# Optimization experiments

Hardware: AMD Instinct MI355X
Metric: run time of the kernel (lower is better)

## Reference

```python
import jax, jax.numpy as jnp
import numpy as np

N, E = 50000, 800000
IN_DIM, HID, HEADS, OUT = 128, 16, 8, 64
SLOPE = 0.2  # DGL GATConv default negative_slope


def setup_inputs() -> dict:
    key = jax.random.key(0)
    ks = jax.random.split(key, 12)
    return {
        "features": jax.random.normal(ks[0], (N, IN_DIM), jnp.float32),
        "src": jax.random.randint(ks[1], (E,), 0, N, jnp.int32),
        "dst": jax.random.randint(ks[2], (E,), 0, N, jnp.int32),
        "w": jax.random.uniform(ks[3], (E,), jnp.float32),
        "W1": jax.random.normal(ks[4], (IN_DIM, HEADS * HID), jnp.float32) / np.sqrt(IN_DIM),
        "al1": jax.random.normal(ks[5], (HEADS, HID), jnp.float32) * 0.1,
        "ar1": jax.random.normal(ks[6], (HEADS, HID), jnp.float32) * 0.1,
        "b1": jnp.zeros((HEADS * HID,), jnp.float32),
        "W2": jax.random.normal(ks[7], (HEADS * HID, OUT), jnp.float32) / np.sqrt(HEADS * HID),
        "al2": jax.random.normal(ks[8], (1, OUT), jnp.float32) * 0.1,
        "ar2": jax.random.normal(ks[9], (1, OUT), jnp.float32) * 0.1,
        "b2": jnp.zeros((OUT,), jnp.float32),
    }


def _gat_layer(x, src, dst, w, W, al, ar, b, heads, dout, act):
    """DGL GATConv with edge_weight: proj -> edge attn -> edge softmax(dst) -> * w -> scatter-sum."""
    n = x.shape[0]
    h = (x @ W).reshape(n, heads, dout)                 # [N,H,D]
    el = (h * al[None]).sum(-1)                         # [N,H] left attn logits
    er = (h * ar[None]).sum(-1)                         # [N,H] right attn logits
    e = el[src] + er[dst]                               # [E,H]
    e = jnp.where(e > 0, e, SLOPE * e)                  # leaky_relu
    m = jax.ops.segment_max(e, dst, num_segments=n)     # per-dst max for stable softmax
    a = jnp.exp(e - m[dst])
    z = jax.ops.segment_sum(a, dst, num_segments=n)
    a = (a / z[dst]) * w[:, None]                       # edge softmax scaled by edge weight
    msg = a[:, :, None] * h[src]                        # [E,H,D] gathered weighted messages
    rst = jax.ops.segment_sum(msg, dst, num_segments=n) # [N,H,D] scatter aggregation
    rst = rst + b.reshape(1, heads, dout)               # GATConv bias
    return act(rst) if act is not None else rst


def reference(features, src, dst, w, W1, al1, ar1, b1, W2, al2, ar2, b2):
    h = _gat_layer(features, src, dst, w, W1, al1, ar1, b1, HEADS, HID, jax.nn.relu)
    h = jax.nn.relu(h).reshape(N, HEADS * HID)          # outer F.relu + flatten(1)
    out = _gat_layer(h, src, dst, w, W2, al2, ar2, b2, 1, OUT, None)
    return out.squeeze(1)                               # [N,OUT]
```

## Files before the change

kernel.cpp:

```cpp
#include <hip/hip_runtime.h>
#include <hip/hip_fp16.h>

#define NN 50000
#define NE 800000

#define NBK 196
#define BSH 8
#define BMASK 255
#define SCAP 5120
#define CHUNK 2048
#define NBLK_A ((NE + CHUNK - 1) / CHUNK)
#define NBLK_P ((NN + 63) / 64)
#define GPAD 4

typedef _Float16 f16x8 __attribute__((ext_vector_type(8)));
typedef float f32x4 __attribute__((ext_vector_type(4)));

__global__ __launch_bounds__(256) void init_k(const float* __restrict__ W1,
                                              const float* __restrict__ W2,
                                              __half* __restrict__ w1t,
                                              __half* __restrict__ w2t,
                                              int* __restrict__ gcur) {
    const int i = blockIdx.x * 256 + threadIdx.x;
    {
        const int k = i >> 7, n = i & 127;
        w1t[n * 128 + k] = __float2half(W1[i]);
    }
    if (i < 128 * 64) {
        const int k = i >> 6, n = i & 63;
        w2t[n * 128 + k] = __float2half(W2[i]);
    }
    if (i < NBK) gcur[i << GPAD] = 0;
}

__global__ __launch_bounds__(256) void sortA_proj1_k(const int* __restrict__ src,
                                                     const int* __restrict__ dst,
                                                     const float* __restrict__ wE,
                                                     int* __restrict__ gcur,
                                                     int2* __restrict__ stage,
                                                     const float* __restrict__ x,
                                                     const __half* __restrict__ w1t,
                                                     const float* __restrict__ al1,
                                                     const float* __restrict__ ar1,
                                                     __half* __restrict__ h1h,
                                                     float* __restrict__ el1,
                                                     float* __restrict__ er1) {
    const int t = threadIdx.x;
    if (blockIdx.x < NBLK_A) {
        __shared__ int hcnt[NBK], lexcl[NBK], lcur[NBK], gbase[NBK];
        __shared__ int wsum[4];
        __shared__ int2 lbuf[CHUNK];
        const int e0 = blockIdx.x * CHUNK;
        const int ne = min(CHUNK, NE - e0);
        if (t < NBK) { hcnt[t] = 0; lcur[t] = 0; }
        __syncthreads();
        for (int i = t; i < ne; i += 256) atomicAdd(&hcnt[dst[e0 + i] >> BSH], 1);
        __syncthreads();
        {
            const int lane = t & 63, wid = t >> 6;
            const int v = (t < NBK) ? hcnt[t] : 0;
            int s = v;
            #pragma unroll
            for (int off = 1; off < 64; off <<= 1) {
                int u = __shfl_up(s, off, 64);
                if (lane >= off) s += u;
            }
            if (lane == 63) wsum[wid] = s;
            __syncthreads();
            int add = 0;
            for (int w = 0; w < wid; w++) add += wsum[w];
            if (t < NBK) lexcl[t] = s - v + add;
        }
        __syncthreads();
        if (t < NBK && hcnt[t] > 0) gbase[t] = atomicAdd(&gcur[t << GPAD], hcnt[t]);
        __syncthreads();
        for (int i = t; i < ne; i += 256) {
            const int d = dst[e0 + i];
            const int b = d >> BSH;
            const int r = atomicAdd(&lcur[b], 1);
            lbuf[lexcl[b] + r] = make_int2((src[e0 + i] & 0xFFFF) | ((d & BMASK) << 16) | (b << 24),
                                           __float_as_int(wE[e0 + i]));
        }
        __syncthreads();
        for (int i = t; i < ne; i += 256) {
            const int2 v = lbuf[i];
            const int b = (unsigned int)v.x >> 24;
            const int pos = gbase[b] + (i - lexcl[b]);
            stage[(size_t)b * SCAP + pos] = v;
        }
    } else {
        const int bid = blockIdx.x - NBLK_A;
        const int l = t & 63, wv = t >> 6;
        const int rbase = bid * 64 + wv * 16;
        const int cl = l & 15, kg = l >> 4;
        const int arow = rbase + cl;
        const float* xrow = x + (size_t)(arow < NN ? arow : NN - 1) * 128;
        f16x8 afrag[4];
        #pragma unroll
        for (int ks = 0; ks < 4; ks++) {
            const float4 u0 = *(const float4*)(xrow + ks * 32 + kg * 8);
            const float4 u1 = *(const float4*)(xrow + ks * 32 + kg * 8 + 4);
            f16x8 a;
            a[0] = (_Float16)u0.x; a[1] = (_Float16)u0.y; a[2] = (_Float16)u0.z; a[3] = (_Float16)u0.w;
            a[4] = (_Float16)u1.x; a[5] = (_Float16)u1.y; a[6] = (_Float16)u1.z; a[7] = (_Float16)u1.w;
            afrag[ks] = a;
        }
        f32x4 acc[8];
        #pragma unroll
        for (int nt = 0; nt < 8; nt++) { acc[nt][0]=0.f; acc[nt][1]=0.f; acc[nt][2]=0.f; acc[nt][3]=0.f; }
        #pragma unroll
        for (int nt = 0; nt < 8; nt++) {
            const f16x8* bp = (const f16x8*)(w1t + (size_t)(nt * 16 + cl) * 128 + kg * 8);
            #pragma unroll
            for (int ks = 0; ks < 4; ks++)
                acc[nt] = __builtin_amdgcn_mfma_f32_16x16x32_f16(afrag[ks], bp[ks * 4], acc[nt], 0, 0, 0);
        }
        const int orow0 = rbase + kg * 4;
        #pragma unroll
        for (int nt = 0; nt < 8; nt++) {
            const int col = nt * 16 + cl;
            const float alc = al1[col], arc = ar1[col];
            #pragma unroll
            for (int r = 0; r < 4; r++) {
                const float v = acc[nt][r];
                const int orow = orow0 + r;
                const bool ok = (orow < NN);
                if (ok) h1h[(size_t)orow * 128 + col] = __float2half(v);
                float pe = v * alc, pr = v * arc;
                #pragma unroll
                for (int m = 1; m < 16; m <<= 1) {
                    pe += __shfl_xor(pe, m, 64);
                    pr += __shfl_xor(pr, m, 64);
                }
                if (ok && cl == 0) {
                    el1[(size_t)orow * 8 + nt] = pe;
                    er1[(size_t)orow * 8 + nt] = pr;
                }
            }
        }
    }
}

__global__ __launch_bounds__(1024) void sortB_k(const int* __restrict__ gcur,
                                                const int2* __restrict__ stage,
                                                int* __restrict__ offs,
                                                unsigned int* __restrict__ csr) {
    __shared__ int cnt[256], cur[256], gall[NBK];
    __shared__ int wsum[4];
    __shared__ int sbase;
    const int b = blockIdx.x, t = threadIdx.x;
    if (t < NBK) gall[t] = gcur[t << GPAD];
    if (t < 256) cnt[t] = 0;
    __syncthreads();
    const int nb = gall[b];
    if (t < 64) {
        int part = 0;
        for (int i = t; i < b; i += 64) part += gall[i];
        #pragma unroll
        for (int m = 1; m < 64; m <<= 1) part += __shfl_xor(part, m, 64);
        if (t == 0) sbase = part;
    }
    const int2* sp = stage + (size_t)b * SCAP;
    for (int i = t; i < nb; i += 1024) atomicAdd(&cnt[(sp[i].x >> 16) & BMASK], 1);
    __syncthreads();
    const int base = sbase;
    const int dlo = b << BSH;
    {
        const int lane = t & 63, wid = t >> 6;
        const int v = (t < 256) ? cnt[t] : 0;
        int s = v;
        #pragma unroll
        for (int off = 1; off < 64; off <<= 1) {
            int u = __shfl_up(s, off, 64);
            if (lane >= off) s += u;
        }
        if (t < 256 && lane == 63) wsum[wid] = s;
        __syncthreads();
        if (t < 256) {
            int add = 0;
            for (int w = 0; w < wid; w++) add += wsum[w];
            const int excl = s - v + add;
            cur[t] = excl;
            if (dlo + t < NN) offs[dlo + t] = base + excl;
        }
        if (b == NBK - 1 && t == 0) offs[NN] = base + nb;
    }
    __syncthreads();
    for (int i = t; i < nb; i += 1024) {
        const int2 pr = sp[i];
        const int dloc = (pr.x >> 16) & BMASK;
        const int sv = pr.x & 0xFFFF;
        const int r = atomicAdd(&cur[dloc], 1);
        const __half hw = __float2half(__int_as_float(pr.y));
        csr[base + r] = (unsigned int)sv | ((unsigned int)__half_as_ushort(hw) << 16);
    }
}

__global__ __launch_bounds__(128) void agg1_k(const int* __restrict__ offs,
                                              const unsigned int* __restrict__ csr,
                                              const __half* __restrict__ h1h,
                                              const float* __restrict__ el1,
                                              const float* __restrict__ er1,
                                              const float* __restrict__ b1,
                                              __half* __restrict__ h2in_h) {
    const int t = threadIdx.x, w = t >> 6, l = t & 63;
    const int n = blockIdx.x * 2 + w;
    const int beg = offs[n], deg = offs[n + 1] - beg;
    const int h = l & 7, eb = l >> 3;
    const int g = l & 15, es = l >> 4, hg = g >> 1;
    const float er_h = er1[(size_t)n * 8 + h];
    float z_lane = 0.f;
    float acc[8];
    #pragma unroll
    for (int j = 0; j < 8; j++) acc[j] = 0.f;
    const float4* hp4 = (const float4*)h1h;

    int pr = 0;
    if (l < 32 && l < deg) pr = (int)csr[beg + l];
    for (int base = 0; base < deg; base += 32) {
        int prn = 0;
        const int nbase = base + 32;
        if (nbase < deg && l < 32 && nbase + l < deg) prn = (int)csr[beg + nbase + l];
        float pwv[4];
        #pragma unroll
        for (int k = 0; k < 4; k++) {
            const unsigned int pre = (unsigned int)__shfl(pr, eb + 8 * k, 64);
            float lg = -1e30f;
            if (base + eb + 8 * k < deg) {
                const float v = el1[(size_t)(pre & 0xFFFF) * 8 + h] + er_h;
                lg = v > 0.f ? v : 0.2f * v;
            }
            const float p = __expf(lg);
            z_lane += p;
            pwv[k] = p * __half2float(__ushort_as_half((unsigned short)(pre >> 16)));
        }
        int sv[8];
        float pp[8];
        #pragma unroll
        for (int k = 0; k < 8; k++) sv[k] = __shfl(pr, es + 4 * k, 64) & 0xFFFF;
        #pragma unroll
        for (int k = 0; k < 8; k++) {
            const int slane = ((es + 4 * (k & 1)) << 3) | hg;
            pp[k] = __shfl(pwv[k >> 1], slane, 64);
        }
        float4 vv[8];
        #pragma unroll
        for (int k = 0; k < 8; k++) vv[k] = hp4[(size_t)sv[k] * 16 + g];
        #pragma unroll
        for (int k = 0; k < 8; k++) {
            #pragma unroll
            for (int q = 0; q < 4; q++) {
                const float2 f = __half22float2(((const __half2*)&vv[k])[q]);
                acc[2 * q]     = fmaf(pp[k], f.x, acc[2 * q]);
                acc[2 * q + 1] = fmaf(pp[k], f.y, acc[2 * q + 1]);
            }
        }
        pr = prn;
    }
    z_lane += __shfl_xor(z_lane, 8, 64);
    z_lane += __shfl_xor(z_lane, 16, 64);
    z_lane += __shfl_xor(z_lane, 32, 64);
    #pragma unroll
    for (int j = 0; j < 8; j++) {
        acc[j] += __shfl_xor(acc[j], 16, 64);
        acc[j] += __shfl_xor(acc[j], 32, 64);
    }
    const float zg = __shfl(z_lane, hg, 64);
    if (l < 16) {
        const float inv = (deg > 0) ? 1.f / zg : 0.f;
        const float4* b4 = (const float4*)b1;
        const float4 bb0 = b4[g * 2], bb1 = b4[g * 2 + 1];
        __half hv[8];
        hv[0] = __float2half(fmaxf(acc[0] * inv + bb0.x, 0.f));
        hv[1] = __float2half(fmaxf(acc[1] * inv + bb0.y, 0.f));
        hv[2] = __float2half(fmaxf(acc[2] * inv + bb0.z, 0.f));
        hv[3] = __float2half(fmaxf(acc[3] * inv + bb0.w, 0.f));
        hv[4] = __float2half(fmaxf(acc[4] * inv + bb1.x, 0.f));
        hv[5] = __float2half(fmaxf(acc[5] * inv + bb1.y, 0.f));
        hv[6] = __float2half(fmaxf(acc[6] * inv + bb1.z, 0.f));
        hv[7] = __float2half(fmaxf(acc[7] * inv + bb1.w, 0.f));
        *(int4*)(h2in_h + (size_t)n * 128 + g * 8) = *(const int4*)hv;
    }
}

__global__ __launch_bounds__(256) void proj2_k(const __half* __restrict__ xh,
                                               const __half* __restrict__ w2t,
                                               const float* __restrict__ al2,
                                               const float* __restrict__ ar2,
                                               __half* __restrict__ h2h,
                                               float* __restrict__ el2,
                                               float* __restrict__ er2) {
    const int t = threadIdx.x, l = t & 63, wv = t >> 6;
    const int rbase = blockIdx.x * 64 + wv * 16;
    const int cl = l & 15, kg = l >> 4;
    const int arow = rbase + cl;
    const __half* xrow = xh + (size_t)(arow < NN ? arow : NN - 1) * 128;
    f16x8 afrag[4];
    #pragma unroll
    for (int ks = 0; ks < 4; ks++)
        afrag[ks] = *(const f16x8*)(xrow + ks * 32 + kg * 8);
    f32x4 acc[4];
    #pragma unroll
    for (int nt = 0; nt < 4; nt++) { acc[nt][0]=0.f; acc[nt][1]=0.f; acc[nt][2]=0.f; acc[nt][3]=0.f; }
    #pragma unroll
    for (int nt = 0; nt < 4; nt++) {
        const f16x8* bp = (const f16x8*)(w2t + (size_t)(nt * 16 + cl) * 128 + kg * 8);
        #pragma unroll
        for (int ks = 0; ks < 4; ks++)
            acc[nt] = __builtin_amdgcn_mfma_f32_16x16x32_f16(afrag[ks], bp[ks * 4], acc[nt], 0, 0, 0);
    }
    const int orow0 = rbase + kg * 4;
    float pe[4] = {0.f, 0.f, 0.f, 0.f}, pr[4] = {0.f, 0.f, 0.f, 0.f};
    #pragma unroll
    for (int nt = 0; nt < 4; nt++) {
        const int col = nt * 16 + cl;
        const float alc = al2[col], arc = ar2[col];
        #pragma unroll
        for (int r = 0; r < 4; r++) {
            const float v = acc[nt][r];
            const int orow = orow0 + r;
            if (orow < NN) h2h[(size_t)orow * 64 + col] = __float2half(v);
            pe[r] = fmaf(v, alc, pe[r]);
            pr[r] = fmaf(v, arc, pr[r]);
        }
    }
    #pragma unroll
    for (int r = 0; r < 4; r++) {
        #pragma unroll
        for (int m = 1; m < 16; m <<= 1) {
            pe[r] += __shfl_xor(pe[r], m, 64);
            pr[r] += __shfl_xor(pr[r], m, 64);
        }
        const int orow = orow0 + r;
        if (cl == 0 && orow < NN) { el2[orow] = pe[r]; er2[orow] = pr[r]; }
    }
}

__global__ __launch_bounds__(128) void agg2_k(const int* __restrict__ offs,
                                              const unsigned int* __restrict__ csr,
                                              const __half* __restrict__ h2h,
                                              const float* __restrict__ el2,
                                              const float* __restrict__ er2,
                                              const float* __restrict__ b2,
                                              float* __restrict__ out) {
    const int t = threadIdx.x, w = t >> 6, l = t & 63;
    const int n = blockIdx.x * 2 + w;
    const int beg = offs[n], deg = offs[n + 1] - beg;
    const int g = l & 7, es = l >> 3;
    const float erd = er2[n];
    float z_lane = 0.f;
    float acc[8];
    #pragma unroll
    for (int j = 0; j < 8; j++) acc[j] = 0.f;
    const float4* hp4 = (const float4*)h2h;

    int pr = 0;
    if (l < 32 && l < deg) pr = (int)csr[beg + l];
    for (int base = 0; base < deg; base += 32) {
        int prn = 0;
        const int nbase = base + 32;
        if (nbase < deg && l < 32 && nbase + l < deg) prn = (int)csr[beg + nbase + l];
        float pw = 0.f;
        if (l < 32 && base + l < deg) {
            const float v = el2[(unsigned int)pr & 0xFFFF] + erd;
            const float lg = v > 0.f ? v : 0.2f * v;
            const float p = __expf(lg);
            z_lane += p;
            pw = p * __half2float(__ushort_as_half((unsigned short)((unsigned int)pr >> 16)));
        }
        int sv[4];
        float pp[4];
        #pragma unroll
        for (int k = 0; k < 4; k++) {
            sv[k] = __shfl(pr, es + 8 * k, 64) & 0xFFFF;
            pp[k] = __shfl(pw, es + 8 * k, 64);
        }
        float4 vv[4];
        #pragma unroll
        for (int k = 0; k < 4; k++) vv[k] = hp4[(size_t)sv[k] * 8 + g];
        #pragma unroll
        for (int k = 0; k < 4; k++) {
            #pragma unroll
            for (int q = 0; q < 4; q++) {
                const float2 f = __half22float2(((const __half2*)&vv[k])[q]);
                acc[2 * q]     = fmaf(pp[k], f.x, acc[2 * q]);
                acc[2 * q + 1] = fmaf(pp[k], f.y, acc[2 * q + 1]);
            }
        }
        pr = prn;
    }
    z_lane += __shfl_xor(z_lane, 1, 64);
    z_lane += __shfl_xor(z_lane, 2, 64);
    z_lane += __shfl_xor(z_lane, 4, 64);
    z_lane += __shfl_xor(z_lane, 8, 64);
    z_lane += __shfl_xor(z_lane, 16, 64);
    z_lane += __shfl_xor(z_lane, 32, 64);
    #pragma unroll
    for (int j = 0; j < 8; j++) {
        acc[j] += __shfl_xor(acc[j], 8, 64);
        acc[j] += __shfl_xor(acc[j], 16, 64);
        acc[j] += __shfl_xor(acc[j], 32, 64);
    }
    if (l < 8) {
        const float inv = (deg > 0) ? 1.f / z_lane : 0.f;
        const float4* b4 = (const float4*)b2;
        const float4 bb0 = b4[g * 2], bb1 = b4[g * 2 + 1];
        float4 o0, o1;
        o0.x = acc[0] * inv + bb0.x;
        o0.y = acc[1] * inv + bb0.y;
        o0.z = acc[2] * inv + bb0.z;
        o0.w = acc[3] * inv + bb0.w;
        o1.x = acc[4] * inv + bb1.x;
        o1.y = acc[5] * inv + bb1.y;
        o1.z = acc[6] * inv + bb1.z;
        o1.w = acc[7] * inv + bb1.w;
        float4* op = (float4*)(out + (size_t)n * 64 + g * 8);
        op[0] = o0; op[1] = o1;
    }
}


extern "C" void kernel_launch(void* const* d_in, const int* in_sizes, int n_in,
                              void* d_out, int out_size, void* d_ws, size_t ws_size,
                              hipStream_t stream) {
    const float* feat = (const float*)d_in[0];
    const int*   srcv = (const int*)d_in[1];
    const int*   dstv = (const int*)d_in[2];
    const float* wE   = (const float*)d_in[3];
    const float* W1   = (const float*)d_in[4];
    const float* al1  = (const float*)d_in[5];
    const float* ar1  = (const float*)d_in[6];
    const float* b1   = (const float*)d_in[7];
    const float* W2   = (const float*)d_in[8];
    const float* al2  = (const float*)d_in[9];
    const float* ar2  = (const float*)d_in[10];
    const float* b2   = (const float*)d_in[11];
    float* out = (float*)d_out;

    char* ws = (char*)d_ws;
    size_t off = 0;
    auto take = [&](size_t bytes) -> char* {
        char* pp = ws + off;
        off = (off + bytes + 255) & ~(size_t)255;
        return pp;
    };
    __half* h1h   = (__half*)take((size_t)NN * 128 * 2);
    __half* h2h   = (__half*)take((size_t)NN * 64 * 2);
    __half* h2in_h= (__half*)take((size_t)NN * 128 * 2);
    float* el1  = (float*)take((size_t)NN * 8 * 4);
    float* er1  = (float*)take((size_t)NN * 8 * 4);
    float* el2  = (float*)take((size_t)NN * 4);
    float* er2  = (float*)take((size_t)NN * 4);
    int* offs   = (int*)take((size_t)(NN + 1) * 4);
    unsigned int* csr = (unsigned int*)take((size_t)NE * 4);
    int* gcur   = (int*)take((size_t)(NBK << GPAD) * 4);
    __half* w1t = (__half*)take((size_t)128 * 128 * 2);
    __half* w2t = (__half*)take((size_t)64 * 128 * 2);
    int2* stage = (int2*)h2in_h;

    init_k<<<64, 256, 0, stream>>>(W1, W2, w1t, w2t, gcur);
    sortA_proj1_k<<<NBLK_A + NBLK_P, 256, 0, stream>>>(srcv, dstv, wE, gcur, stage,
                                                       feat, w1t, al1, ar1, h1h, el1, er1);
    sortB_k<<<NBK, 1024, 0, stream>>>(gcur, stage, offs, csr);
    agg1_k<<<NN / 2, 128, 0, stream>>>(offs, csr, h1h, el1, er1, b1, h2in_h);
    proj2_k<<<(NN + 63) / 64, 256, 0, stream>>>(h2in_h, w2t, al2, ar2, h2h, el2, er2);
    agg2_k<<<NN / 2, 128, 0, stream>>>(offs, csr, h2h, el2, er2, b2, out);
}
```

Before: 138.0 us.

## Precompute layer-1 edge attention weights and softmax denominators during CSR sort

Moves the layer-1 per-edge exp(leaky_relu(el+er))*w computation into the CSR scatter kernel. It writes per-edge fp16 weights for all 8 heads and per-node denominators, accumulated with shared-memory atomics. The aggregation kernel then just reads the precomputed weights instead of gathering el1 and computing exponentials. This adds an extra per-edge array write and read, and it puts more work into a low-occupancy sort kernel with shared atomic contention.

```diff
diff --git a/kernel.cpp b/kernel.cpp
--- a/kernel.cpp
+++ b/kernel.cpp
@@ -143,14 +143,26 @@
 
 __global__ __launch_bounds__(1024) void sortB_k(const int* __restrict__ gcur,
                                                 const int2* __restrict__ stage,
+                                                const float* __restrict__ el1,
+                                                const float* __restrict__ er1,
                                                 int* __restrict__ offs,
-                                                unsigned int* __restrict__ csr) {
+                                                unsigned int* __restrict__ csr,
+                                                __half* __restrict__ pwh,
+                                                float* __restrict__ zf) {
     __shared__ int cnt[256], cur[256], gall[NBK];
     __shared__ int wsum[4];
     __shared__ int sbase;
+    __shared__ float erl[256][8];
+    __shared__ float zacc[256][8];
     const int b = blockIdx.x, t = threadIdx.x;
+    const int dlo = b << BSH;
     if (t < NBK) gall[t] = gcur[t << GPAD];
     if (t < 256) cnt[t] = 0;
+    for (int i = t; i < 2048; i += 1024) {
+        const int node = dlo + (i >> 3);
+        erl[i >> 3][i & 7] = (node < NN) ? er1[(size_t)node * 8 + (i & 7)] : 0.f;
+        zacc[i >> 3][i & 7] = 0.f;
+    }
     __syncthreads();
     const int nb = gall[b];
     if (t < 64) {
@@ -164,7 +176,6 @@
     for (int i = t; i < nb; i += 1024) atomicAdd(&cnt[(sp[i].x >> 16) & BMASK], 1);
     __syncthreads();
     const int base = sbase;
-    const int dlo = b << BSH;
     {
         const int lane = t & 63, wid = t >> 6;
         const int v = (t < 256) ? cnt[t] : 0;
@@ -190,58 +201,60 @@
         const int2 pr = sp[i];
         const int dloc = (pr.x >> 16) & BMASK;
         const int sv = pr.x & 0xFFFF;
+        const float wf = __int_as_float(pr.y);
         const int r = atomicAdd(&cur[dloc], 1);
-        const __half hw = __float2half(__int_as_float(pr.y));
+        const __half hw = __float2half(wf);
         csr[base + r] = (unsigned int)sv | ((unsigned int)__half_as_ushort(hw) << 16);
+        const float4 e0v = *(const float4*)(el1 + (size_t)sv * 8);
+        const float4 e1v = *(const float4*)(el1 + (size_t)sv * 8 + 4);
+        float elv[8];
+        elv[0]=e0v.x; elv[1]=e0v.y; elv[2]=e0v.z; elv[3]=e0v.w;
+        elv[4]=e1v.x; elv[5]=e1v.y; elv[6]=e1v.z; elv[7]=e1v.w;
+        __half hv[8];
+        #pragma unroll
+        for (int h = 0; h < 8; h++) {
+            float lg = elv[h] + erl[dloc][h];
+            lg = lg > 0.f ? lg : 0.2f * lg;
+            const float p = __expf(lg);
+            atomicAdd(&zacc[dloc][h], p);
+            hv[h] = __float2half(p * wf);
+        }
+        *(int4*)(pwh + (size_t)(base + r) * 8) = *(const int4*)hv;
+    }
+    __syncthreads();
+    for (int i = t; i < 2048; i += 1024) {
+        const int node = dlo + (i >> 3);
+        if (node < NN) zf[(size_t)node * 8 + (i & 7)] = zacc[i >> 3][i & 7];
     }
 }
 
 __global__ __launch_bounds__(128) void agg1_k(const int* __restrict__ offs,
                                               const unsigned int* __restrict__ csr,
+                                              const __half* __restrict__ pwh,
+                                              const float* __restrict__ zf,
                                               const __half* __restrict__ h1h,
-                                              const float* __restrict__ el1,
-                                              const float* __restrict__ er1,
                                               const float* __restrict__ b1,
                                               __half* __restrict__ h2in_h) {
     const int t = threadIdx.x, w = t >> 6, l = t & 63;
     const int n = blockIdx.x * 2 + w;
     const int beg = offs[n], deg = offs[n + 1] - beg;
-    const int h = l & 7, eb = l >> 3;
     const int g = l & 15, es = l >> 4, hg = g >> 1;
-    const float er_h = er1[(size_t)n * 8 + h];
-    float z_lane = 0.f;
     float acc[8];
     #pragma unroll
     for (int j = 0; j < 8; j++) acc[j] = 0.f;
     const float4* hp4 = (const float4*)h1h;
 
-    int pr = 0;
-    if (l < 32 && l < deg) pr = (int)csr[beg + l];
     for (int base = 0; base < deg; base += 32) {
-        int prn = 0;
-        const int nbase = base + 32;
-        if (nbase < deg && l < 32 && nbase + l < deg) prn = (int)csr[beg + nbase + l];
-        float pwv[4];
-        #pragma unroll
-        for (int k = 0; k < 4; k++) {
-            const unsigned int pre = (unsigned int)__shfl(pr, eb + 8 * k, 64);
-            float lg = -1e30f;
-            if (base + eb + 8 * k < deg) {
-                const float v = el1[(size_t)(pre & 0xFFFF) * 8 + h] + er_h;
-                lg = v > 0.f ? v : 0.2f * v;
-            }
-            const float p = __expf(lg);
-            z_lane += p;
-            pwv[k] = p * __half2float(__ushort_as_half((unsigned short)(pre >> 16)));
-        }
         int sv[8];
         float pp[8];
         #pragma unroll
-        for (int k = 0; k < 8; k++) sv[k] = __shfl(pr, es + 4 * k, 64) & 0xFFFF;
-        #pragma unroll
         for (int k = 0; k < 8; k++) {
-            const int slane = ((es + 4 * (k & 1)) << 3) | hg;
-            pp[k] = __shfl(pwv[k >> 1], slane, 64);
+            const int E = es + 4 * k;
+            const bool ok = (base + E < deg);
+            const int idx = beg + base + (ok ? E : 0);
+            const unsigned int c = csr[idx];
+            sv[k] = ok ? (int)(c & 0xFFFF) : 0;
+            pp[k] = ok ? __half2float(pwh[(size_t)idx * 8 + hg]) : 0.f;
         }
         float4 vv[8];
         #pragma unroll
@@ -255,19 +268,15 @@
                 acc[2 * q + 1] = fmaf(pp[k], f.y, acc[2 * q + 1]);
             }
         }
-        pr = prn;
-    }
-    z_lane += __shfl_xor(z_lane, 8, 64);
-    z_lane += __shfl_xor(z_lane, 16, 64);
-    z_lane += __shfl_xor(z_lane, 32, 64);
+    }
     #pragma unroll
     for (int j = 0; j < 8; j++) {
         acc[j] += __shfl_xor(acc[j], 16, 64);
         acc[j] += __shfl_xor(acc[j], 32, 64);
     }
-    const float zg = __shfl(z_lane, hg, 64);
     if (l < 16) {
-        const float inv = (deg > 0) ? 1.f / zg : 0.f;
+        const float z = zf[(size_t)n * 8 + hg];
+        const float inv = (deg > 0) ? 1.f / z : 0.f;
         const float4* b4 = (const float4*)b1;
         const float4 bb0 = b4[g * 2], bb1 = b4[g * 2 + 1];
         __half hv[8];
@@ -456,13 +465,15 @@
     int* gcur   = (int*)take((size_t)(NBK << GPAD) * 4);
     __half* w1t = (__half*)take((size_t)128 * 128 * 2);
     __half* w2t = (__half*)take((size_t)64 * 128 * 2);
+    __half* pwh = (__half*)take((size_t)NE * 8 * 2);
+    float* zf   = (float*)take((size_t)NN * 8 * 4);
     int2* stage = (int2*)h2in_h;
 
     init_k<<<64, 256, 0, stream>>>(W1, W2, w1t, w2t, gcur);
     sortA_proj1_k<<<NBLK_A + NBLK_P, 256, 0, stream>>>(srcv, dstv, wE, gcur, stage,
                                                        feat, w1t, al1, ar1, h1h, el1, er1);
-    sortB_k<<<NBK, 1024, 0, stream>>>(gcur, stage, offs, csr);
-    agg1_k<<<NN / 2, 128, 0, stream>>>(offs, csr, h1h, el1, er1, b1, h2in_h);
+    sortB_k<<<NBK, 1024, 0, stream>>>(gcur, stage, el1, er1, offs, csr, pwh, zf);
+    agg1_k<<<NN / 2, 128, 0, stream>>>(offs, csr, pwh, zf, h1h, b1, h2in_h);
     proj2_k<<<(NN + 63) / 64, 256, 0, stream>>>(h2in_h, w2t, al2, ar2, h2h, el2, er2);
     agg2_k<<<NN / 2, 128, 0, stream>>>(offs, csr, h2h, el2, er2, b2, out);
 }
```

After: 189.3 us. 1.37x slower.

## Process two destination nodes per wavefront in both aggregation kernels

Applied to the files above, without the earlier changes.

Each wavefront in agg1_k and agg2_k now handles two destination nodes together, 16 edges per node per iteration, instead of one node at 32 edges per iteration. The change targets wasted lanes when average degree (~16) is below the old 32-edge chunk, and aims to keep more gathers in flight per wave. The grid is halved to match. Costs: more registers for two accumulator sets, loop length bound by the larger degree of the pair, and the next-chunk CSR prefetch has been dropped.

```diff
diff --git a/kernel.cpp b/kernel.cpp
--- a/kernel.cpp
+++ b/kernel.cpp
@@ -15,6 +15,10 @@
 
 typedef _Float16 f16x8 __attribute__((ext_vector_type(8)));
 typedef float f32x4 __attribute__((ext_vector_type(4)));
+
+__device__ __forceinline__ float h2f_hi(unsigned int u) {
+    return __half2float(__ushort_as_half((unsigned short)(u >> 16)));
+}
 
 __global__ __launch_bounds__(256) void init_k(const float* __restrict__ W1,
                                               const float* __restrict__ W2,
@@ -204,81 +208,109 @@
                                               const float* __restrict__ b1,
                                               __half* __restrict__ h2in_h) {
     const int t = threadIdx.x, w = t >> 6, l = t & 63;
-    const int n = blockIdx.x * 2 + w;
-    const int beg = offs[n], deg = offs[n + 1] - beg;
-    const int h = l & 7, eb = l >> 3;
+    const int nA = blockIdx.x * 4 + w * 2;
+    const int nB = nA + 1;
+    const int begA = offs[nA], degA = offs[nA + 1] - begA;
+    const int begB = offs[nB], degB = offs[nB + 1] - begB;
+    const int h = l & 7, e0 = l >> 3, e1 = e0 + 8;
     const int g = l & 15, es = l >> 4, hg = g >> 1;
-    const float er_h = er1[(size_t)n * 8 + h];
-    float z_lane = 0.f;
-    float acc[8];
-    #pragma unroll
-    for (int j = 0; j < 8; j++) acc[j] = 0.f;
+    const float erA = er1[(size_t)nA * 8 + h];
+    const float erB = er1[(size_t)nB * 8 + h];
+    float zA = 0.f, zB = 0.f;
+    float accA[8], accB[8];
+    #pragma unroll
+    for (int j = 0; j < 8; j++) { accA[j] = 0.f; accB[j] = 0.f; }
     const float4* hp4 = (const float4*)h1h;
-
-    int pr = 0;
-    if (l < 32 && l < deg) pr = (int)csr[beg + l];
-    for (int base = 0; base < deg; base += 32) {
-        int prn = 0;
-        const int nbase = base + 32;
-        if (nbase < deg && l < 32 && nbase + l < deg) prn = (int)csr[beg + nbase + l];
-        float pwv[4];
-        #pragma unroll
-        for (int k = 0; k < 4; k++) {
-            const unsigned int pre = (unsigned int)__shfl(pr, eb + 8 * k, 64);
-            float lg = -1e30f;
-            if (base + eb + 8 * k < deg) {
-                const float v = el1[(size_t)(pre & 0xFFFF) * 8 + h] + er_h;
-                lg = v > 0.f ? v : 0.2f * v;
-            }
-            const float p = __expf(lg);
-            z_lane += p;
-            pwv[k] = p * __half2float(__ushort_as_half((unsigned short)(pre >> 16)));
-        }
-        int sv[8];
-        float pp[8];
-        #pragma unroll
-        for (int k = 0; k < 8; k++) sv[k] = __shfl(pr, es + 4 * k, 64) & 0xFFFF;
-        #pragma unroll
-        for (int k = 0; k < 8; k++) {
-            const int slane = ((es + 4 * (k & 1)) << 3) | hg;
-            pp[k] = __shfl(pwv[k >> 1], slane, 64);
-        }
-        float4 vv[8];
-        #pragma unroll
-        for (int k = 0; k < 8; k++) vv[k] = hp4[(size_t)sv[k] * 16 + g];
-        #pragma unroll
-        for (int k = 0; k < 8; k++) {
-            #pragma unroll
-            for (int q = 0; q < 4; q++) {
-                const float2 f = __half22float2(((const __half2*)&vv[k])[q]);
-                acc[2 * q]     = fmaf(pp[k], f.x, acc[2 * q]);
-                acc[2 * q + 1] = fmaf(pp[k], f.y, acc[2 * q + 1]);
-            }
-        }
-        pr = prn;
-    }
-    z_lane += __shfl_xor(z_lane, 8, 64);
-    z_lane += __shfl_xor(z_lane, 16, 64);
-    z_lane += __shfl_xor(z_lane, 32, 64);
+    const int dmax = max(degA, degB);
+
+    for (int base = 0; base < dmax; base += 16) {
+        int pr = 0;
+        if (l < 16) { if (base + l < degA) pr = (int)csr[begA + base + l]; }
+        else if (l < 32) { const int e = l - 16; if (base + e < degB) pr = (int)csr[begB + base + e]; }
+        const unsigned int pA0 = (unsigned int)__shfl(pr, e0, 64);
+        const unsigned int pA1 = (unsigned int)__shfl(pr, e1, 64);
+        const unsigned int pB0 = (unsigned int)__shfl(pr, 16 + e0, 64);
+        const unsigned int pB1 = (unsigned int)__shfl(pr, 16 + e1, 64);
+        float lgA0 = -1e30f, lgA1 = -1e30f, lgB0 = -1e30f, lgB1 = -1e30f;
+        if (base + e0 < degA) { const float v = el1[(size_t)(pA0 & 0xFFFF) * 8 + h] + erA; lgA0 = v > 0.f ? v : 0.2f * v; }
+        if (base + e1 < degA) { const float v = el1[(size_t)(pA1 & 0xFFFF) * 8 + h] + erA; lgA1 = v > 0.f ? v : 0.2f * v; }
+        if (base + e0 < degB) { const float v = el1[(size_t)(pB0 & 0xFFFF) * 8 + h] + erB; lgB0 = v > 0.f ? v : 0.2f * v; }
+        if (base + e1 < degB) { const float v = el1[(size_t)(pB1 & 0xFFFF) * 8 + h] + erB; lgB1 = v > 0.f ? v : 0.2f * v; }
+        const float eA0 = __expf(lgA0), eA1 = __expf(lgA1);
+        const float eB0 = __expf(lgB0), eB1 = __expf(lgB1);
+        zA += eA0 + eA1;
+        zB += eB0 + eB1;
+        const float pwA0 = eA0 * h2f_hi(pA0), pwA1 = eA1 * h2f_hi(pA1);
+        const float pwB0 = eB0 * h2f_hi(pB0), pwB1 = eB1 * h2f_hi(pB1);
+        const int sA0 = __shfl(pr, es, 64) & 0xFFFF;
+        const int sA1 = __shfl(pr, es + 4, 64) & 0xFFFF;
+        const int sA2 = __shfl(pr, es + 8, 64) & 0xFFFF;
+        const int sA3 = __shfl(pr, es + 12, 64) & 0xFFFF;
+        const int sB0 = __shfl(pr, 16 + es, 64) & 0xFFFF;
+        const int sB1 = __shfl(pr, 16 + es + 4, 64) & 0xFFFF;
+        const int sB2 = __shfl(pr, 16 + es + 8, 64) & 0xFFFF;
+        const int sB3 = __shfl(pr, 16 + es + 12, 64) & 0xFFFF;
+        const float qA0 = __shfl(pwA0, es * 8 + hg, 64);
+        const float qA1 = __shfl(pwA0, (es + 4) * 8 + hg, 64);
+        const float qA2 = __shfl(pwA1, es * 8 + hg, 64);
+        const float qA3 = __shfl(pwA1, (es + 4) * 8 + hg, 64);
+        const float qB0 = __shfl(pwB0, es * 8 + hg, 64);
+        const float qB1 = __shfl(pwB0, (es + 4) * 8 + hg, 64);
+        const float qB2 = __shfl(pwB1, es * 8 + hg, 64);
+        const float qB3 = __shfl(pwB1, (es + 4) * 8 + hg, 64);
+        const float4 vA0 = hp4[(size_t)sA0 * 16 + g];
+        const float4 vA1 = hp4[(size_t)sA1 * 16 + g];
+        const float4 vA2 = hp4[(size_t)sA2 * 16 + g];
+        const float4 vA3 = hp4[(size_t)sA3 * 16 + g];
+        const float4 vB0 = hp4[(size_t)sB0 * 16 + g];
+        const float4 vB1 = hp4[(size_t)sB1 * 16 + g];
+        const float4 vB2 = hp4[(size_t)sB2 * 16 + g];
+        const float4 vB3 = hp4[(size_t)sB3 * 16 + g];
+        #pragma unroll
+        for (int q = 0; q < 4; q++) {
+            const float2 fA0 = __half22float2(((const __half2*)&vA0)[q]);
+            const float2 fA1 = __half22float2(((const __half2*)&vA1)[q]);
+            const float2 fA2 = __half22float2(((const __half2*)&vA2)[q]);
+            const float2 fA3 = __half22float2(((const __half2*)&vA3)[q]);
+            accA[2 * q]     = fmaf(qA0, fA0.x, fmaf(qA1, fA1.x, fmaf(qA2, fA2.x, fmaf(qA3, fA3.x, accA[2 * q]))));
+            accA[2 * q + 1] = fmaf(qA0, fA0.y, fmaf(qA1, fA1.y, fmaf(qA2, fA2.y, fmaf(qA3, fA3.y, accA[2 * q + 1]))));
+            const float2 fB0 = __half22float2(((const __half2*)&vB0)[q]);
+            const float2 fB1 = __half22float2(((const __half2*)&vB1)[q]);
+            const float2 fB2 = __half22float2(((const __half2*)&vB2)[q]);
+            const float2 fB3 = __half22float2(((const __half2*)&vB3)[q]);
+            accB[2 * q]     = fmaf(qB0, fB0.x, fmaf(qB1, fB1.x, fmaf(qB2, fB2.x, fmaf(qB3, fB3.x, accB[2 * q]))));
+            accB[2 * q + 1] = fmaf(qB0, fB0.y, fmaf(qB1, fB1.y, fmaf(qB2, fB2.y, fmaf(qB3, fB3.y, accB[2 * q + 1]))));
+        }
+    }
+    zA += __shfl_xor(zA, 8, 64);  zA += __shfl_xor(zA, 16, 64);  zA += __shfl_xor(zA, 32, 64);
+    zB += __shfl_xor(zB, 8, 64);  zB += __shfl_xor(zB, 16, 64);  zB += __shfl_xor(zB, 32, 64);
     #pragma unroll
     for (int j = 0; j < 8; j++) {
-        acc[j] += __shfl_xor(acc[j], 16, 64);
-        acc[j] += __shfl_xor(acc[j], 32, 64);
-    }
-    const float zg = __shfl(z_lane, hg, 64);
-    if (l < 16) {
+        accA[j] += __shfl_xor(accA[j], 16, 64);
+        accA[j] += __shfl_xor(accA[j], 32, 64);
+        accB[j] += __shfl_xor(accB[j], 16, 64);
+        accB[j] += __shfl_xor(accB[j], 32, 64);
+    }
+    const float zgA = __shfl(zA, hg, 64);
+    const float zgB = __shfl(zB, hg, 64);
+    const float4* b4 = (const float4*)b1;
+    const float4 bb0 = b4[g * 2], bb1 = b4[g * 2 + 1];
+    if (l < 32) {
+        const bool isA = (l < 16);
+        const int n = isA ? nA : nB;
+        const int deg = isA ? degA : degB;
+        const float zg = isA ? zgA : zgB;
+        const float* ac = isA ? accA : accB;
         const float inv = (deg > 0) ? 1.f / zg : 0.f;
-        const float4* b4 = (const float4*)b1;
-        const float4 bb0 = b4[g * 2], bb1 = b4[g * 2 + 1];
         __half hv[8];
-        hv[0] = __float2half(fmaxf(acc[0] * inv + bb0.x, 0.f));
-        hv[1] = __float2half(fmaxf(acc[1] * inv + bb0.y, 0.f));
-        hv[2] = __float2half(fmaxf(acc[2] * inv + bb0.z, 0.f));
-        hv[3] = __float2half(fmaxf(acc[3] * inv + bb0.w, 0.f));
-        hv[4] = __float2half(fmaxf(acc[4] * inv + bb1.x, 0.f));
-        hv[5] = __float2half(fmaxf(acc[5] * inv + bb1.y, 0.f));
-        hv[6] = __float2half(fmaxf(acc[6] * inv + bb1.z, 0.f));
-        hv[7] = __float2half(fmaxf(acc[7] * inv + bb1.w, 0.f));
+        hv[0] = __float2half(fmaxf(ac[0] * inv + bb0.x, 0.f));
+        hv[1] = __float2half(fmaxf(ac[1] * inv + bb0.y, 0.f));
+        hv[2] = __float2half(fmaxf(ac[2] * inv + bb0.z, 0.f));
+        hv[3] = __float2half(fmaxf(ac[3] * inv + bb0.w, 0.f));
+        hv[4] = __float2half(fmaxf(ac[4] * inv + bb1.x, 0.f));
+        hv[5] = __float2half(fmaxf(ac[5] * inv + bb1.y, 0.f));
+        hv[6] = __float2half(fmaxf(ac[6] * inv + bb1.z, 0.f));
+        hv[7] = __float2half(fmaxf(ac[7] * inv + bb1.w, 0.f));
         *(int4*)(h2in_h + (size_t)n * 128 + g * 8) = *(const int4*)hv;
     }
 }
@@ -344,76 +376,90 @@
                                               const float* __restrict__ b2,
                                               float* __restrict__ out) {
     const int t = threadIdx.x, w = t >> 6, l = t & 63;
-    const int n = blockIdx.x * 2 + w;
-    const int beg = offs[n], deg = offs[n + 1] - beg;
+    const int nA = blockIdx.x * 4 + w * 2;
+    const int nB = nA + 1;
+    const int begA = offs[nA], degA = offs[nA + 1] - begA;
+    const int begB = offs[nB], degB = offs[nB + 1] - begB;
     const int g = l & 7, es = l >> 3;
-    const float erd = er2[n];
-    float z_lane = 0.f;
-    float acc[8];
-    #pragma unroll
-    for (int j = 0; j < 8; j++) acc[j] = 0.f;
+    const float erdA = er2[nA], erdB = er2[nB];
+    float zl = 0.f;
+    float accA[8], accB[8];
+    #pragma unroll
+    for (int j = 0; j < 8; j++) { accA[j] = 0.f; accB[j] = 0.f; }
     const float4* hp4 = (const float4*)h2h;
-
-    int pr = 0;
-    if (l < 32 && l < deg) pr = (int)csr[beg + l];
-    for (int base = 0; base < deg; base += 32) {
-        int prn = 0;
-        const int nbase = base + 32;
-        if (nbase < deg && l < 32 && nbase + l < deg) prn = (int)csr[beg + nbase + l];
+    const int dmax = max(degA, degB);
+
+    for (int base = 0; base < dmax; base += 16) {
+        int pr = 0;
+        bool okE = false;
+        if (l < 16) { okE = (base + l < degA); if (okE) pr = (int)csr[begA + base + l]; }
+        else if (l < 32) { const int e = l - 16; okE = (base + e < degB); if (okE) pr = (int)csr[begB + base + e]; }
         float pw = 0.f;
-        if (l < 32 && base + l < deg) {
-            const float v = el2[(unsigned int)pr & 0xFFFF] + erd;
+        if (okE) {
+            const float er = (l < 16) ? erdA : erdB;
+            const float v = el2[(unsigned int)pr & 0xFFFF] + er;
             const float lg = v > 0.f ? v : 0.2f * v;
             const float p = __expf(lg);
-            z_lane += p;
-            pw = p * __half2float(__ushort_as_half((unsigned short)((unsigned int)pr >> 16)));
-        }
-        int sv[4];
-        float pp[4];
-        #pragma unroll
-        for (int k = 0; k < 4; k++) {
-            sv[k] = __shfl(pr, es + 8 * k, 64) & 0xFFFF;
-            pp[k] = __shfl(pw, es + 8 * k, 64);
-        }
-        float4 vv[4];
-        #pragma unroll
-        for (int k = 0; k < 4; k++) vv[k] = hp4[(size_t)sv[k] * 8 + g];
-        #pragma unroll
-        for (int k = 0; k < 4; k++) {
-            #pragma unroll
-            for (int q = 0; q < 4; q++) {
-                const float2 f = __half22float2(((const __half2*)&vv[k])[q]);
-                acc[2 * q]     = fmaf(pp[k], f.x, acc[2 * q]);
-                acc[2 * q + 1] = fmaf(pp[k], f.y, acc[2 * q + 1]);
-            }
-        }
-        pr = prn;
-    }
-    z_lane += __shfl_xor(z_lane, 1, 64);
-    z_lane += __shfl_xor(z_lane, 2, 64);
-    z_lane += __shfl_xor(z_lane, 4, 64);
-    z_lane += __shfl_xor(z_lane, 8, 64);
-    z_lane += __shfl_xor(z_lane, 16, 64);
-    z_lane += __shfl_xor(z_lane, 32, 64);
+            zl += p;
+            pw = p * h2f_hi((unsigned int)pr);
+        }
+        const int sA0 = __shfl(pr, es, 64) & 0xFFFF;
+        const int sA1 = __shfl(pr, es + 8, 64) & 0xFFFF;
+        const int sB0 = __shfl(pr, 16 + es, 64) & 0xFFFF;
+        const int sB1 = __shfl(pr, 16 + es + 8, 64) & 0xFFFF;
+        const float qA0 = __shfl(pw, es, 64);
+        const float qA1 = __shfl(pw, es + 8, 64);
+        const float qB0 = __shfl(pw, 16 + es, 64);
+        const float qB1 = __shfl(pw, 16 + es + 8, 64);
+        const float4 vA0 = hp4[(size_t)sA0 * 8 + g];
+        const float4 vA1 = hp4[(size_t)sA1 * 8 + g];
+        const float4 vB0 = hp4[(size_t)sB0 * 8 + g];
+        const float4 vB1 = hp4[(size_t)sB1 * 8 + g];
+        #pragma unroll
+        for (int q = 0; q < 4; q++) {
+            const float2 fA0 = __half22float2(((const __half2*)&vA0)[q]);
+            const float2 fA1 = __half22float2(((const __half2*)&vA1)[q]);
+            accA[2 * q]     = fmaf(qA0, fA0.x, fmaf(qA1, fA1.x, accA[2 * q]));
+            accA[2 * q + 1] = fmaf(qA0, fA0.y, fmaf(qA1, fA1.y, accA[2 * q + 1]));
+            const float2 fB0 = __half22float2(((const __half2*)&vB0)[q]);
+            const float2 fB1 = __half22float2(((const __half2*)&vB1)[q]);
+            accB[2 * q]     = fmaf(qB0, fB0.x, fmaf(qB1, fB1.x, accB[2 * q]));
+            accB[2 * q + 1] = fmaf(qB0, fB0.y, fmaf(qB1, fB1.y, accB[2 * q + 1]));
+        }
+    }
+    zl += __shfl_xor(zl, 1, 64);
+    zl += __shfl_xor(zl, 2, 64);
+    zl += __shfl_xor(zl, 4, 64);
+    zl += __shfl_xor(zl, 8, 64);
+    const float zA = __shfl(zl, 0, 64);
+    const float zB = __shfl(zl, 16, 64);
     #pragma unroll
     for (int j = 0; j < 8; j++) {
-        acc[j] += __shfl_xor(acc[j], 8, 64);
-        acc[j] += __shfl_xor(acc[j], 16, 64);
-        acc[j] += __shfl_xor(acc[j], 32, 64);
-    }
-    if (l < 8) {
-        const float inv = (deg > 0) ? 1.f / z_lane : 0.f;
-        const float4* b4 = (const float4*)b2;
-        const float4 bb0 = b4[g * 2], bb1 = b4[g * 2 + 1];
+        accA[j] += __shfl_xor(accA[j], 8, 64);
+        accA[j] += __shfl_xor(accA[j], 16, 64);
+        accA[j] += __shfl_xor(accA[j], 32, 64);
+        accB[j] += __shfl_xor(accB[j], 8, 64);
+        accB[j] += __shfl_xor(accB[j], 16, 64);
+        accB[j] += __shfl_xor(accB[j], 32, 64);
+    }
+    const float4* b4 = (const float4*)b2;
+    const float4 bb0 = b4[g * 2], bb1 = b4[g * 2 + 1];
+    if (l < 8 || (l >= 16 && l < 24)) {
+        const bool isA = (l < 8);
+        const int n = isA ? nA : nB;
+        const int deg = isA ? degA : degB;
+        const float z = isA ? zA : zB;
+        const float* ac = isA ? accA : accB;
+        const float inv = (deg > 0) ? 1.f / z : 0.f;
         float4 o0, o1;
-        o0.x = acc[0] * inv + bb0.x;
-        o0.y = acc[1] * inv + bb0.y;
-        o0.z = acc[2] * inv + bb0.z;
-        o0.w = acc[3] * inv + bb0.w;
-        o1.x = acc[4] * inv + bb1.x;
-        o1.y = acc[5] * inv + bb1.y;
-        o1.z = acc[6] * inv + bb1.z;
-        o1.w = acc[7] * inv + bb1.w;
+        o0.x = ac[0] * inv + bb0.x;
+        o0.y = ac[1] * inv + bb0.y;
+        o0.z = ac[2] * inv + bb0.z;
+        o0.w = ac[3] * inv + bb0.w;
+        o1.x = ac[4] * inv + bb1.x;
+        o1.y = ac[5] * inv + bb1.y;
+        o1.z = ac[6] * inv + bb1.z;
+        o1.w = ac[7] * inv + bb1.w;
         float4* op = (float4*)(out + (size_t)n * 64 + g * 8);
         op[0] = o0; op[1] = o1;
     }
@@ -462,7 +508,7 @@
     sortA_proj1_k<<<NBLK_A + NBLK_P, 256, 0, stream>>>(srcv, dstv, wE, gcur, stage,
                                                        feat, w1t, al1, ar1, h1h, el1, er1);
     sortB_k<<<NBK, 1024, 0, stream>>>(gcur, stage, offs, csr);
-    agg1_k<<<NN / 2, 128, 0, stream>>>(offs, csr, h1h, el1, er1, b1, h2in_h);
+    agg1_k<<<NN / 4, 128, 0, stream>>>(offs, csr, h1h, el1, er1, b1, h2in_h);
     proj2_k<<<(NN + 63) / 64, 256, 0, stream>>>(h2in_h, w2t, al2, ar2, h2h, el2, er2);
-    agg2_k<<<NN / 2, 128, 0, stream>>>(offs, csr, h2h, el2, er2, b2, out);
-}
+    agg2_k<<<NN / 4, 128, 0, stream>>>(offs, csr, h2h, el2, er2, b2, out);
+}
```

After: 163.3 us. 18.3% more time.
